# Performance work log

Measured on AMD Instinct MI355X. Metric: run time of the kernel, lower is better.

Reference implementation:

```python
import jax, jax.numpy as jnp
import numpy as np

H, DK, DV, DEMB = 16, 64, 64, 1024
D_MODEL = H * DV


def setup_inputs() -> dict:
    key = jax.random.key(0)
    ks = jax.random.split(key, 9)
    scale = 0.02
    x = jax.random.normal(ks[0], (4, 2048, DEMB), dtype=jnp.float32)
    wq = jax.random.normal(ks[1], (DEMB, H * DK), dtype=jnp.float32) * scale
    bq = jnp.zeros((H * DK,), dtype=jnp.float32)
    wk = jax.random.normal(ks[2], (DEMB, H * DK), dtype=jnp.float32) * scale
    bk = jnp.zeros((H * DK,), dtype=jnp.float32)
    wv = jax.random.normal(ks[3], (DEMB, H * DV), dtype=jnp.float32) * scale
    bv = jnp.zeros((H * DV,), dtype=jnp.float32)
    wo = jax.random.normal(ks[4], (D_MODEL, D_MODEL), dtype=jnp.float32) * scale
    bo = jnp.zeros((D_MODEL,), dtype=jnp.float32)
    return {"x": x, "wq": wq, "bq": bq, "wk": wk, "bk": bk,
            "wv": wv, "bv": bv, "wo": wo, "bo": bo, "mask": 0}


def _split_heads(t, h):
    # (b, s, h*d) -> (b, h, s, d)
    b, s, _ = t.shape
    return t.reshape(b, s, h, -1).transpose(0, 2, 1, 3)


def reference(x, wq, bq, wk, bk, wv, bv, wo, bo, mask):
    b, s, _ = x.shape
    qs = _split_heads(x @ wq + bq, H)  # (b, h, s, dk)
    ks = _split_heads(x @ wk + bk, H)
    vs = _split_heads(x @ wv + bv, H)  # (b, h, s, dv)
    # FAITHFUL quirk: original scales by 1/sqrt(len(ks[0])) == 1/sqrt(n_heads),
    # not 1/sqrt(d_k).
    scores = jnp.einsum('bhqd,bhkd->bhqk', qs, ks) / jnp.sqrt(jnp.float32(H))
    # FAITHFUL quirk: masked_fill(mask == 0, ...) with scalar bool mask is a
    # no-op (True == 0 is False), so no masking is ever applied.
    attn = jax.nn.softmax(scores, axis=-1)
    out = jnp.einsum('bhqk,bhkd->bhqd', attn, vs)  # (b, h, s, dv)
    out = out.transpose(0, 2, 1, 3).reshape(b, s, D_MODEL)
    return out @ wo + bo
```

## Files before the change

### kernel.cpp

```cpp
#include <hip/hip_runtime.h>
#include <stdint.h>

typedef __attribute__((ext_vector_type(8))) short short8;
typedef __attribute__((ext_vector_type(4))) short short4v;
typedef __attribute__((ext_vector_type(4))) float floatx4;
typedef __attribute__((ext_vector_type(4))) _Float16 half4;
typedef __attribute__((ext_vector_type(2))) __fp16 pk2;

#define SEQ 2048
#define NTOK 8192
#define QSCALE 0.360673760222241f

#define MFMA16F16(a,b,c) __builtin_amdgcn_mfma_f32_16x16x16f16((a),(b),(c),0,0,0)

__device__ __forceinline__ float b2f(unsigned short u){
  union { unsigned int i; float f; } v; v.i = ((unsigned int)u) << 16; return v.f;
}
__device__ __forceinline__ unsigned short f2b(float f){
  union { float f; unsigned int i; } v; v.f = f;
  unsigned int r = v.i + 0x7fffu + ((v.i >> 16) & 1u);
  return (unsigned short)(r >> 16);
}
__device__ __forceinline__ void async16(const unsigned short* g, unsigned short* l){
  __builtin_amdgcn_global_load_lds(
      (const __attribute__((address_space(1))) unsigned int*)g,
      (__attribute__((address_space(3))) unsigned int*)l, 16, 0, 0);
}

__global__ __launch_bounds__(256) void prep_kernel(
    const float* __restrict__ x,
    const float* __restrict__ wq, const float* __restrict__ wk,
    const float* __restrict__ wv, const float* __restrict__ wo,
    const float* __restrict__ bq, const float* __restrict__ bk,
    const float* __restrict__ bv,
    unsigned short* __restrict__ xb,
    unsigned short* __restrict__ wqkvT, unsigned short* __restrict__ woT,
    float* __restrict__ bqkv)
{
  __shared__ unsigned short lT[64][72];
  const int bid = blockIdx.x;
  const int tid = threadIdx.x;
  if (bid < 8192){
    int i = (bid*256 + tid)*4;
    float4 v = *(const float4*)(x + i);
    short4v o;
    o[0] = (short)f2b(v.x); o[1] = (short)f2b(v.y);
    o[2] = (short)f2b(v.z); o[3] = (short)f2b(v.w);
    *(short4v*)(xb + i) = o;
  } else if (bid < 9216){
    int idx = bid - 8192;
    int sel = idx >> 8, rest = idx & 255;
    const float* src = (sel==0)?wq:(sel==1)?wk:(sel==2)?wv:wo;
    unsigned short* dst = (sel<3) ? (wqkvT + (size_t)sel*1024*1024) : woT;
    int n0 = (rest & 15) * 64, k0 = (rest >> 4) * 64;
#pragma unroll
    for (int i=0;i<4;i++){
      int ch = tid + i*256;
      int r = ch>>4, c = (ch&15)*4;
      float4 v = *(const float4*)(src + (size_t)(k0+r)*1024 + n0 + c);
      lT[r][c+0] = f2b(v.x); lT[r][c+1] = f2b(v.y);
      lT[r][c+2] = f2b(v.z); lT[r][c+3] = f2b(v.w);
    }
    __syncthreads();
#pragma unroll
    for (int i=0;i<2;i++){
      int ch = tid + i*256;
      int rn = ch>>3, c = (ch&7)*8;
      short8 v;
#pragma unroll
      for (int j=0;j<8;j++) v[j] = (short)lT[c+j][rn];
      *(short8*)(dst + (size_t)(n0+rn)*1024 + k0 + c) = v;
    }
  } else {
    int i = (bid - 9216)*256 + tid;
    if (i < 3072){
      int sel = i >> 10, j = i & 1023;
      bqkv[i] = (sel==0)?bq[j]:(sel==1)?bk[j]:bv[j];
    }
  }
}

template<int OUT_F32, int SCALE_Q>
__global__ __launch_bounds__(256) void gemm_bt_kernel(
    const unsigned short* __restrict__ A,
    const unsigned short* __restrict__ Bt,
    const float* __restrict__ bias,
    void* __restrict__ Cv,
    int M, int N, int K)
{
  __shared__ unsigned short lA[128*64];
  __shared__ unsigned short lB[128*64];
  const int tid  = threadIdx.x;
  const int lane = tid & 63;
  const int wave = tid >> 6;
  const int quad = lane >> 4;
  const int l15  = lane & 15;
  const int wR = (wave >> 1) * 64;
  const int wC = (wave & 1) * 64;
  const int rowB = blockIdx.y * 128;
  const int colB = blockIdx.x * 128;

  const int srow = wave*32 + (lane>>3);
  const int sc8  = (lane&7) ^ (lane>>3);
  const unsigned short* gA = A  + (size_t)(rowB + srow)*K + sc8*8;
  const unsigned short* gB = Bt + (size_t)(colB + srow)*K + sc8*8;
  unsigned short* lAw = lA + wave*32*64 + lane*8;
  unsigned short* lBw = lB + wave*32*64 + lane*8;

  floatx4 acc[4][4];
#pragma unroll
  for (int t=0;t<4;t++)
#pragma unroll
    for (int u=0;u<4;u++) acc[t][u] = (floatx4){0.f,0.f,0.f,0.f};

  for (int kt = 0; kt < K; kt += 64){
    __syncthreads();
#pragma unroll
    for (int i=0;i<4;i++){
      async16(gA + (size_t)i*8*K + kt, lAw + i*512);
      async16(gB + (size_t)i*8*K + kt, lBw + i*512);
    }
    __syncthreads();
#pragma unroll
    for (int ks=0; ks<2; ks++){
      const int cph = ((ks*4 + quad) ^ (l15 & 7)) * 8;
      short8 af[4], bf[4];
#pragma unroll
      for (int t=0;t<4;t++) af[t] = *(const short8*)&lA[(wR + t*16 + l15)*64 + cph];
#pragma unroll
      for (int u=0;u<4;u++) bf[u] = *(const short8*)&lB[(wC + u*16 + l15)*64 + cph];
#pragma unroll
      for (int t=0;t<4;t++)
#pragma unroll
        for (int u=0;u<4;u++)
          acc[t][u] = __builtin_amdgcn_mfma_f32_16x16x32_bf16(af[t], bf[u], acc[t][u], 0, 0, 0);
    }
  }
#pragma unroll
  for (int u=0;u<4;u++){
    int col = colB + wC + u*16 + l15;
    float bval = bias[col];
    float scale = (SCALE_Q && col < 1024) ? QSCALE : 1.0f;
#pragma unroll
    for (int t=0;t<4;t++){
      int row0 = rowB + wR + t*16 + quad*4;
#pragma unroll
      for (int r=0;r<4;r++){
        float val = (acc[t][u][r] + bval) * scale;
        if (OUT_F32) ((float*)Cv)[(size_t)(row0 + r)*N + col] = val;
        else ((unsigned short*)Cv)[(size_t)(row0 + r)*N + col] = f2b(val);
      }
    }
  }
}

__global__ __launch_bounds__(256) void transpose_v_kernel(
    const unsigned short* __restrict__ qkv,
    unsigned short* __restrict__ vt)
{
  __shared__ unsigned short lT[64][72];
  const int bh = blockIdx.x;
  const int b = bh >> 4, h = bh & 15;
  const int s0 = blockIdx.y * 64;
  const int tid = threadIdx.x;
#pragma unroll
  for (int i=0;i<2;i++){
    int ch = tid + i*256;
    int r = ch >> 3, c = (ch & 7)*8;
    short8 raw = *(const short8*)(qkv + (size_t)(b*SEQ + s0 + r)*3072 + 2048 + h*64 + c);
#pragma unroll
    for (int j=0;j<8;j++){
      union { _Float16 h; unsigned short u; } cv;
      cv.h = (_Float16)b2f((unsigned short)raw[j]);
      lT[r][c+j] = cv.u;
    }
  }
  __syncthreads();
#pragma unroll
  for (int i=0;i<2;i++){
    int ch = tid + i*256;
    int dv = ch >> 3, c = (ch & 7)*8;
    short8 v;
#pragma unroll
    for (int j=0;j<8;j++) v[j] = (short)lT[c+j][dv];
    *(short8*)(vt + (size_t)(bh*64 + dv)*2048 + s0 + c) = v;
  }
}

__global__ __launch_bounds__(256) void flash_attn_kernel(
    const unsigned short* __restrict__ qkv,
    const unsigned short* __restrict__ vt,
    unsigned short* __restrict__ attn_out)
{
  __shared__ unsigned short sK[2][64*64];
  __shared__ _Float16 sV[2][64*64];
  const int bh = blockIdx.x;
  const int b = bh >> 4, h = bh & 15;
  const int qt = blockIdx.y;
  const int tid = threadIdx.x;
  const int wave = tid >> 6;
  const int lane = tid & 63;
  const int quad = lane >> 4, l15 = lane & 15;
  const int tok0 = b*SEQ + qt*128;

  const int srow = lane >> 3;
  const int sc8  = (lane & 7) ^ srow;
  const unsigned short* gK = qkv + (size_t)(b*SEQ + wave*16 + srow)*3072 + 1024 + h*64 + sc8*8;
  const unsigned short* gV = vt  + (size_t)(bh*64 + wave*16 + srow)*2048 + sc8*8;
  const int ldso = (wave*16)*64 + lane*8;

  short8 qf[2][2];
#pragma unroll
  for (int t=0;t<2;t++)
#pragma unroll
    for (int ks=0;ks<2;ks++)
      qf[t][ks] = *(const short8*)(qkv + (size_t)(tok0 + wave*32 + t*16 + l15)*3072
                                   + h*64 + ks*32 + quad*8);

  floatx4 oacc[2][4];
  float psum[2] = {0.f, 0.f};
#pragma unroll
  for (int t=0;t<2;t++)
#pragma unroll
    for (int v=0;v<4;v++) oacc[t][v] = (floatx4){0.f,0.f,0.f,0.f};

#pragma unroll
  for (int i=0;i<2;i++){
    async16(gK + (size_t)i*8*3072, &sK[0][ldso + i*512]);
    async16(gV + (size_t)i*8*2048, (unsigned short*)&sV[0][ldso + i*512]);
  }
  __syncthreads();

  for (int it = 0; it < SEQ/64; it++){
    const int bi = it & 1;
    if (it + 1 < SEQ/64){
      const int nx = (it + 1) * 64;
#pragma unroll
      for (int i=0;i<2;i++){
        async16(gK + (size_t)(i*8 + (size_t)nx)*3072, &sK[bi^1][ldso + i*512]);
        async16(gV + (size_t)i*8*2048 + nx, (unsigned short*)&sV[bi^1][ldso + i*512]);
      }
    }

    floatx4 sacc[4][2];
#pragma unroll
    for (int u=0;u<4;u++)
#pragma unroll
      for (int t=0;t<2;t++) sacc[u][t] = (floatx4){0.f,0.f,0.f,0.f};
#pragma unroll
    for (int ks=0;ks<2;ks++){
      const int cph = ((ks*4 + quad) ^ (l15 & 7)) * 8;
      short8 kf[4];
#pragma unroll
      for (int u=0;u<4;u++) kf[u] = *(const short8*)&sK[bi][(u*16 + l15)*64 + cph];
#pragma unroll
      for (int u=0;u<4;u++)
#pragma unroll
        for (int t=0;t<2;t++)
          sacc[u][t] = __builtin_amdgcn_mfma_f32_16x16x32_bf16(kf[u], qf[t][ks], sacc[u][t], 0,0,0);
    }

    half4 pf[4][2];
#pragma unroll
    for (int t=0;t<2;t++){
#pragma unroll
      for (int u=0;u<4;u++){
        float p0 = __builtin_amdgcn_exp2f(sacc[u][t][0]);
        float p1 = __builtin_amdgcn_exp2f(sacc[u][t][1]);
        float p2 = __builtin_amdgcn_exp2f(sacc[u][t][2]);
        float p3 = __builtin_amdgcn_exp2f(sacc[u][t][3]);
        psum[t] += (p0+p1)+(p2+p3);
        union { pk2 p2v[2]; half4 h4; } cv;
        cv.p2v[0] = __builtin_amdgcn_cvt_pkrtz(p0,p1);
        cv.p2v[1] = __builtin_amdgcn_cvt_pkrtz(p2,p3);
        pf[u][t] = cv.h4;
      }
    }

#pragma unroll
    for (int v=0;v<4;v++){
      half4 vf[4];
#pragma unroll
      for (int u=0;u<4;u++){
        const int cph = ((2*u + (quad>>1)) ^ (l15 & 7)) * 8 + (quad&1)*4;
        vf[u] = *(const half4*)&sV[bi][(v*16 + l15)*64 + cph];
      }
#pragma unroll
      for (int t=0;t<2;t++)
#pragma unroll
        for (int u=0;u<4;u++)
          oacc[t][v] = MFMA16F16(pf[u][t], vf[u], oacc[t][v]);
    }
    __syncthreads();
  }

#pragma unroll
  for (int t=0;t<2;t++){
    float s = psum[t];
    s += __shfl_xor(s, 16);
    s += __shfl_xor(s, 32);
    psum[t] = s;
  }
#pragma unroll
  for (int t=0;t<2;t++){
#pragma unroll
    for (int r=0;r<4;r++){
      float inv = 1.0f / __shfl(psum[t], quad*4 + r);
      int tok = tok0 + wave*32 + t*16 + quad*4 + r;
#pragma unroll
      for (int v=0;v<4;v++)
        attn_out[(size_t)tok*1024 + h*64 + v*16 + l15] = f2b(oacc[t][v][r] * inv);
    }
  }
}

extern "C" void kernel_launch(void* const* d_in, const int* in_sizes, int n_in,
                              void* d_out, int out_size, void* d_ws, size_t ws_size,
                              hipStream_t stream)
{
  const float* x  = (const float*)d_in[0];
  const float* wq = (const float*)d_in[1];
  const float* bq = (const float*)d_in[2];
  const float* wk = (const float*)d_in[3];
  const float* bk = (const float*)d_in[4];
  const float* wv = (const float*)d_in[5];
  const float* bv = (const float*)d_in[6];
  const float* wo = (const float*)d_in[7];
  const float* bo = (const float*)d_in[8];
  float* out = (float*)d_out;

  char* ws = (char*)d_ws;
  unsigned short* wqkvT  = (unsigned short*)(ws);
  unsigned short* woT    = (unsigned short*)(ws + 6291456);
  float*          bqkv   = (float*)(ws + 8388608);
  unsigned short* xb     = (unsigned short*)(ws + 8400896);
  unsigned short* qkvbuf = (unsigned short*)(ws + 25178112);
  unsigned short* vtbuf  = (unsigned short*)(ws + 75509760);
  unsigned short* aobuf  = (unsigned short*)(ws + 92286976);

  prep_kernel<<<dim3(9228), 256, 0, stream>>>(x, wq, wk, wv, wo, bq, bk, bv,
                                              xb, wqkvT, woT, bqkv);
  gemm_bt_kernel<0,1><<<dim3(24, 64), 256, 0, stream>>>(xb, wqkvT, bqkv, qkvbuf, 8192, 3072, 1024);
  transpose_v_kernel<<<dim3(64, 32), 256, 0, stream>>>(qkvbuf, vtbuf);
  flash_attn_kernel<<<dim3(64, 16), 256, 0, stream>>>(qkvbuf, vtbuf, aobuf);
  gemm_bt_kernel<1,0><<<dim3(8, 64), 256, 0, stream>>>(aobuf, woT, bo, out, 8192, 1024, 1024);
}
```

Measured before the change: 314.9 us.

## Split-K output GEMM with atomics and register-staged attention K/V tiles

The output projection GEMM is split along K into two slices, doubling the grid, with results accumulated into a zeroed fp32 output through atomicAdd. Only the first slice adds the bias, and a memset is added before the chain. The flash attention kernel drops the double-buffered async global-to-LDS loads. It now prefetches the next K/V tile into registers and writes it to padded single-buffer LDS, with V rearranged at store time so the PV fragment comes from one 16-byte read. This trades the async-copy pipeline for explicit register prefetch, and adds atomic traffic plus an extra memset in exchange for more parallelism in the last GEMM.

```diff
diff --git a/kernel.cpp b/kernel.cpp
--- a/kernel.cpp
+++ b/kernel.cpp
@@ -80,13 +80,13 @@
   }
 }
 
-template<int OUT_F32, int SCALE_Q>
+template<int OUT_MODE, int SCALE_Q>
 __global__ __launch_bounds__(256) void gemm_bt_kernel(
     const unsigned short* __restrict__ A,
     const unsigned short* __restrict__ Bt,
     const float* __restrict__ bias,
     void* __restrict__ Cv,
-    int M, int N, int K)
+    int M, int N, int K, int Klen)
 {
   __shared__ unsigned short lA[128*64];
   __shared__ unsigned short lB[128*64];
@@ -99,6 +99,7 @@
   const int wC = (wave & 1) * 64;
   const int rowB = blockIdx.y * 128;
   const int colB = blockIdx.x * 128;
+  const int kt0  = blockIdx.z * Klen;
 
   const int srow = wave*32 + (lane>>3);
   const int sc8  = (lane&7) ^ (lane>>3);
@@ -113,7 +114,7 @@
 #pragma unroll
     for (int u=0;u<4;u++) acc[t][u] = (floatx4){0.f,0.f,0.f,0.f};
 
-  for (int kt = 0; kt < K; kt += 64){
+  for (int kt = kt0; kt < kt0 + Klen; kt += 64){
     __syncthreads();
 #pragma unroll
     for (int i=0;i<4;i++){
@@ -139,7 +140,7 @@
 #pragma unroll
   for (int u=0;u<4;u++){
     int col = colB + wC + u*16 + l15;
-    float bval = bias[col];
+    float bval = (OUT_MODE == 2 && blockIdx.z != 0) ? 0.f : bias[col];
     float scale = (SCALE_Q && col < 1024) ? QSCALE : 1.0f;
 #pragma unroll
     for (int t=0;t<4;t++){
@@ -147,7 +148,7 @@
 #pragma unroll
       for (int r=0;r<4;r++){
         float val = (acc[t][u][r] + bval) * scale;
-        if (OUT_F32) ((float*)Cv)[(size_t)(row0 + r)*N + col] = val;
+        if (OUT_MODE == 2)      atomicAdd(&((float*)Cv)[(size_t)(row0 + r)*N + col], val);
         else ((unsigned short*)Cv)[(size_t)(row0 + r)*N + col] = f2b(val);
       }
     }
@@ -192,8 +193,8 @@
     const unsigned short* __restrict__ vt,
     unsigned short* __restrict__ attn_out)
 {
-  __shared__ unsigned short sK[2][64*64];
-  __shared__ _Float16 sV[2][64*64];
+  __shared__ unsigned short sK[64][72];
+  __shared__ unsigned short sVt[64][72];
   const int bh = blockIdx.x;
   const int b = bh >> 4, h = bh & 15;
   const int qt = blockIdx.y;
@@ -203,12 +204,6 @@
   const int quad = lane >> 4, l15 = lane & 15;
   const int tok0 = b*SEQ + qt*128;
 
-  const int srow = lane >> 3;
-  const int sc8  = (lane & 7) ^ srow;
-  const unsigned short* gK = qkv + (size_t)(b*SEQ + wave*16 + srow)*3072 + 1024 + h*64 + sc8*8;
-  const unsigned short* gV = vt  + (size_t)(bh*64 + wave*16 + srow)*2048 + sc8*8;
-  const int ldso = (wave*16)*64 + lane*8;
-
   short8 qf[2][2];
 #pragma unroll
   for (int t=0;t<2;t++)
@@ -224,22 +219,37 @@
 #pragma unroll
     for (int v=0;v<4;v++) oacc[t][v] = (floatx4){0.f,0.f,0.f,0.f};
 
-#pragma unroll
-  for (int i=0;i<2;i++){
-    async16(gK + (size_t)i*8*3072, &sK[0][ldso + i*512]);
-    async16(gV + (size_t)i*8*2048, (unsigned short*)&sV[0][ldso + i*512]);
-  }
-  __syncthreads();
+  const int ch0 = tid, ch1 = tid + 256;
+  const int r0 = ch0 >> 3, c0 = (ch0 & 7)*8;
+  const int r1 = ch1 >> 3, c1 = (ch1 & 7)*8;
+  const int u0 = c0 >> 4, qd0 = (c0 & 15) >> 2;
+  const int u1 = c1 >> 4, qd1 = (c1 & 15) >> 2;
+  short8 rk[2], rv[2];
+  rk[0] = *(const short8*)(qkv + (size_t)(b*SEQ + r0)*3072 + 1024 + h*64 + c0);
+  rk[1] = *(const short8*)(qkv + (size_t)(b*SEQ + r1)*3072 + 1024 + h*64 + c1);
+  rv[0] = *(const short8*)(vt  + (size_t)(bh*64 + r0)*2048 + c0);
+  rv[1] = *(const short8*)(vt  + (size_t)(bh*64 + r1)*2048 + c1);
 
   for (int it = 0; it < SEQ/64; it++){
-    const int bi = it & 1;
+    __syncthreads();
+    *(short8*)&sK[r0][c0] = rk[0];
+    *(short8*)&sK[r1][c1] = rk[1];
+    { short4v lo = {rv[0][0],rv[0][1],rv[0][2],rv[0][3]};
+      short4v hi = {rv[0][4],rv[0][5],rv[0][6],rv[0][7]};
+      *(short4v*)&sVt[r0][qd0*16 + u0*4]     = lo;
+      *(short4v*)&sVt[r0][(qd0+1)*16 + u0*4] = hi;
+      lo = (short4v){rv[1][0],rv[1][1],rv[1][2],rv[1][3]};
+      hi = (short4v){rv[1][4],rv[1][5],rv[1][6],rv[1][7]};
+      *(short4v*)&sVt[r1][qd1*16 + u1*4]     = lo;
+      *(short4v*)&sVt[r1][(qd1+1)*16 + u1*4] = hi;
+    }
+    __syncthreads();
     if (it + 1 < SEQ/64){
-      const int nx = (it + 1) * 64;
-#pragma unroll
-      for (int i=0;i<2;i++){
-        async16(gK + (size_t)(i*8 + (size_t)nx)*3072, &sK[bi^1][ldso + i*512]);
-        async16(gV + (size_t)i*8*2048 + nx, (unsigned short*)&sV[bi^1][ldso + i*512]);
-      }
+      int itn = (it + 1) * 64;
+      rk[0] = *(const short8*)(qkv + (size_t)(b*SEQ + itn + r0)*3072 + 1024 + h*64 + c0);
+      rk[1] = *(const short8*)(qkv + (size_t)(b*SEQ + itn + r1)*3072 + 1024 + h*64 + c1);
+      rv[0] = *(const short8*)(vt  + (size_t)(bh*64 + r0)*2048 + itn + c0);
+      rv[1] = *(const short8*)(vt  + (size_t)(bh*64 + r1)*2048 + itn + c1);
     }
 
     floatx4 sacc[4][2];
@@ -249,10 +259,9 @@
       for (int t=0;t<2;t++) sacc[u][t] = (floatx4){0.f,0.f,0.f,0.f};
 #pragma unroll
     for (int ks=0;ks<2;ks++){
-      const int cph = ((ks*4 + quad) ^ (l15 & 7)) * 8;
       short8 kf[4];
 #pragma unroll
-      for (int u=0;u<4;u++) kf[u] = *(const short8*)&sK[bi][(u*16 + l15)*64 + cph];
+      for (int u=0;u<4;u++) kf[u] = *(const short8*)&sK[u*16 + l15][ks*32 + quad*8];
 #pragma unroll
       for (int u=0;u<4;u++)
 #pragma unroll
@@ -281,9 +290,13 @@
     for (int v=0;v<4;v++){
       half4 vf[4];
 #pragma unroll
-      for (int u=0;u<4;u++){
-        const int cph = ((2*u + (quad>>1)) ^ (l15 & 7)) * 8 + (quad&1)*4;
-        vf[u] = *(const half4*)&sV[bi][(v*16 + l15)*64 + cph];
+      for (int hh=0;hh<2;hh++){
+        short8 w = *(const short8*)&sVt[v*16 + l15][quad*16 + hh*8];
+        union { short4v s; half4 h; } a, bb;
+        a.s  = (short4v){w[0],w[1],w[2],w[3]};
+        bb.s = (short4v){w[4],w[5],w[6],w[7]};
+        vf[2*hh]   = a.h;
+        vf[2*hh+1] = bb.h;
       }
 #pragma unroll
       for (int t=0;t<2;t++)
@@ -291,7 +304,6 @@
         for (int u=0;u<4;u++)
           oacc[t][v] = MFMA16F16(pf[u][t], vf[u], oacc[t][v]);
     }
-    __syncthreads();
   }
 
 #pragma unroll
@@ -338,10 +350,13 @@
   unsigned short* vtbuf  = (unsigned short*)(ws + 75509760);
   unsigned short* aobuf  = (unsigned short*)(ws + 92286976);
 
+  hipMemsetAsync(out, 0, (size_t)out_size * sizeof(float), stream);
   prep_kernel<<<dim3(9228), 256, 0, stream>>>(x, wq, wk, wv, wo, bq, bk, bv,
                                               xb, wqkvT, woT, bqkv);
-  gemm_bt_kernel<0,1><<<dim3(24, 64), 256, 0, stream>>>(xb, wqkvT, bqkv, qkvbuf, 8192, 3072, 1024);
+  gemm_bt_kernel<0,1><<<dim3(24, 64), 256, 0, stream>>>(xb, wqkvT, bqkv, qkvbuf,
+                                                        8192, 3072, 1024, 1024);
   transpose_v_kernel<<<dim3(64, 32), 256, 0, stream>>>(qkvbuf, vtbuf);
   flash_attn_kernel<<<dim3(64, 16), 256, 0, stream>>>(qkvbuf, vtbuf, aobuf);
-  gemm_bt_kernel<1,0><<<dim3(8, 64), 256, 0, stream>>>(aobuf, woT, bo, out, 8192, 1024, 1024);
-}
+  gemm_bt_kernel<2,0><<<dim3(8, 64, 2), 256, 0, stream>>>(aobuf, woT, bo, out,
+                                                          8192, 1024, 1024, 512);
+}
```

Measured after the change: 345.0 us. 1.1x slower.
